# Optimization experiments

Measured on AMD Instinct MI355X. Metric: run time of the kernel, lower is better.

The kernel has to match this reference:

```python
import jax, jax.numpy as jnp
import numpy as np

B, T, D = 16, 4096, 768
S_MAX = 128  # max sentence (segment) count per sample


def setup_inputs() -> dict:
    key = jax.random.key(0)
    ks = jax.random.split(key, 8)
    hidden = jax.random.normal(ks[0], (B, T, D), dtype=jnp.float32)
    # sorted per-token segment ids == cumulative torch.split span structure
    seg_ids = jnp.sort(jax.random.randint(ks[1], (B, T), 0, S_MAX, dtype=jnp.int32), axis=-1)
    s1, s2, s3 = 1.0 / np.sqrt(D), 1.0 / np.sqrt(384), 1.0 / np.sqrt(128)
    W1 = jax.random.normal(ks[2], (D, 384), dtype=jnp.float32) * s1
    b1 = jnp.zeros((384,), dtype=jnp.float32)
    W2 = jax.random.normal(ks[3], (384, 128), dtype=jnp.float32) * s2
    b2 = jnp.zeros((128,), dtype=jnp.float32)
    W3 = jax.random.normal(ks[4], (128, 2), dtype=jnp.float32) * s3
    b3 = jnp.zeros((2,), dtype=jnp.float32)
    return {"hidden": hidden, "seg_ids": seg_ids, "W1": W1, "b1": b1,
            "W2": W2, "b2": b2, "W3": W3, "b3": b3}


def reference(hidden, seg_ids, W1, b1, W2, b2, W3, b3):
    # split_tensor: per-sample segment-sum over token spans, padded to S_MAX.
    # Segments with no tokens come out zero, matching F.pad of the torch code.
    sent_em = jax.vmap(
        lambda h, s: jax.ops.segment_sum(h, s, num_segments=S_MAX)
    )(hidden, seg_ids)  # [B, S_MAX, D]
    # sent_pred MLP head
    x = jax.nn.relu(jnp.einsum('bsd,df->bsf', sent_em, W1) + b1)
    x = jax.nn.relu(jnp.einsum('bsf,fg->bsg', x, W2) + b2)
    pred = jnp.einsum('bsg,gc->bsc', x, W3) + b3  # [B, S_MAX, 2]
    return pred.reshape(B * S_MAX, -1)
```

## Files before the change

### kernel.cpp

```cpp
#include <hip/hip_runtime.h>

#define BATCH 16
#define TOK   4096
#define DIM   768
#define SMAX  128
#define BM    8

typedef float f32x4 __attribute__((ext_vector_type(4)));
typedef short s16x8 __attribute__((ext_vector_type(8)));

__device__ __forceinline__ int lower_bound_i(const int* __restrict__ a, int n, int v) {
    int lo = 0, hi = n;
    while (lo < hi) {
        int m = (lo + hi) >> 1;
        if (a[m] < v) lo = m + 1; else hi = m;
    }
    return lo;
}

__device__ __forceinline__ float f4get(const float4& v, int k) {
    switch (k) {
        case 0: return v.x;
        case 1: return v.y;
        case 2: return v.z;
        default: return v.w;
    }
}

__device__ __forceinline__ void f4acc(float4& a, const float4& v) {
    a.x += v.x; a.y += v.y; a.z += v.z; a.w += v.w;
}

__device__ __forceinline__ unsigned short bf16_rne(float f) {
    unsigned int u = __float_as_uint(f);
    u += 0x7FFFu + ((u >> 16) & 1u);
    return (unsigned short)(u >> 16);
}

__device__ __forceinline__ unsigned int bf16_pack2(float f0, float f1) {
    unsigned int u0 = __float_as_uint(f0) + 0x8000u;
    unsigned int u1 = __float_as_uint(f1) + 0x8000u;
    return (u0 >> 16) | (u1 & 0xFFFF0000u);
}

__global__ __launch_bounds__(768)
void prep_w1t_kernel(const float* __restrict__ W1, unsigned short* __restrict__ W1T) {
    const int c = blockIdx.x;
    const int k = threadIdx.x;
    W1T[c * 768 + k] = bf16_rne(W1[(size_t)k * 384 + c]);
}

__global__ __launch_bounds__(192)
void bounds_kernel(const int* __restrict__ seg, int* __restrict__ bounds) {
    const int b = blockIdx.x;
    const int s = threadIdx.x;
    if (s <= SMAX)
        bounds[b * (SMAX + 1) + s] = lower_bound_i(seg + b * TOK, TOK, s);
}

__global__ __launch_bounds__(1024)
void fused_kernel(const float* __restrict__ hidden,
                  const int* __restrict__ bounds,
                  const unsigned short* __restrict__ W1T, const float* __restrict__ b1,
                  const float* __restrict__ W2, const float* __restrict__ b2,
                  const float* __restrict__ W3, const float* __restrict__ b3,
                  float* __restrict__ out) {
    __shared__ __align__(16) unsigned int A_bf32[16 * 388];
    __shared__ __align__(16) float X1[BM * 384];
    __shared__ __align__(16) float X2[BM * 128];
    __shared__ __align__(16) float P2[8 * BM * 128];

    const int tid  = threadIdx.x;
    const int row0 = blockIdx.x * BM;
    const int b    = row0 / SMAX;
    const int s0   = row0 % SMAX;
    const int grp  = tid >> 7;
    const int lane = tid & 127;
    const int h    = lane >> 6;
    const int l6   = lane & 63;

    for (int i = tid; i < 8 * 388; i += 1024)
        A_bf32[8 * 388 + i] = 0u;

    {
        const int lo = bounds[b * (SMAX + 1) + s0 + grp];
        const int hi = bounds[b * (SMAX + 1) + s0 + grp + 1];

        const float4* __restrict__ hp =
            reinterpret_cast<const float4*>(hidden + (size_t)b * TOK * DIM) + l6 * 3;

        float4 a0 = make_float4(0.f, 0.f, 0.f, 0.f);
        float4 a1 = make_float4(0.f, 0.f, 0.f, 0.f);
        float4 a2 = make_float4(0.f, 0.f, 0.f, 0.f);

        int t = lo + h;
        for (; t + 8 <= hi; t += 8) {
            float4 v0[4], v1[4], v2[4];
            #pragma unroll
            for (int u = 0; u < 4; ++u) {
                const float4* p = hp + (size_t)(t + 2 * u) * 192;
                v0[u] = p[0]; v1[u] = p[1]; v2[u] = p[2];
            }
            #pragma unroll
            for (int u = 0; u < 4; ++u) {
                f4acc(a0, v0[u]); f4acc(a1, v1[u]); f4acc(a2, v2[u]);
            }
        }
        for (; t < hi; t += 2) {
            const float4* p = hp + (size_t)t * 192;
            f4acc(a0, p[0]); f4acc(a1, p[1]); f4acc(a2, p[2]);
        }

        float4* scr = reinterpret_cast<float4*>(P2) + (grp * 64 + l6) * 3;
        if (h == 1) {
            scr[0] = a0; scr[1] = a1; scr[2] = a2;
        }
        __syncthreads();
        if (h == 0) {
            f4acc(a0, scr[0]); f4acc(a1, scr[1]); f4acc(a2, scr[2]);
            const int base = grp * 388 + l6 * 6;
            A_bf32[base + 0] = bf16_pack2(a0.x, a0.y);
            A_bf32[base + 1] = bf16_pack2(a0.z, a0.w);
            A_bf32[base + 2] = bf16_pack2(a1.x, a1.y);
            A_bf32[base + 3] = bf16_pack2(a1.z, a1.w);
            A_bf32[base + 4] = bf16_pack2(a2.x, a2.y);
            A_bf32[base + 5] = bf16_pack2(a2.z, a2.w);
        }
    }
    __syncthreads();

    {
        const int wid  = tid >> 6;
        const int l    = tid & 63;
        const int lrow = l & 15;
        const int lg   = l >> 4;

        if (wid < 12) {
            const int n0 = wid * 32;
            const int n1 = n0 + 16;
            f32x4 acc0 = {0.f, 0.f, 0.f, 0.f};
            f32x4 acc1 = {0.f, 0.f, 0.f, 0.f};

            const unsigned int* abase = &A_bf32[lrow * 388 + lg * 4];
            const unsigned short* w0p = W1T + (size_t)(n0 + lrow) * 768 + lg * 8;
            const unsigned short* w1p = W1T + (size_t)(n1 + lrow) * 768 + lg * 8;

            for (int ks = 0; ks < 24; ++ks) {
                s16x8 af  = *reinterpret_cast<const s16x8*>(abase + ks * 16);
                s16x8 bf0 = *reinterpret_cast<const s16x8*>(w0p + ks * 32);
                s16x8 bf1 = *reinterpret_cast<const s16x8*>(w1p + ks * 32);
                acc0 = __builtin_amdgcn_mfma_f32_16x16x32_bf16(af, bf0, acc0, 0, 0, 0);
                acc1 = __builtin_amdgcn_mfma_f32_16x16x32_bf16(af, bf1, acc1, 0, 0, 0);
            }

            if (lg < 2) {
                const int c0  = n0 + lrow;
                const int c1c = n1 + lrow;
                const float bb0 = b1[c0];
                const float bb1 = b1[c1c];
                #pragma unroll
                for (int r4 = 0; r4 < 4; ++r4) {
                    const int row = lg * 4 + r4;
                    const float v0 = acc0[r4] + bb0;
                    const float v1 = acc1[r4] + bb1;
                    X1[row * 384 + c0]  = v0 > 0.f ? v0 : 0.f;
                    X1[row * 384 + c1c] = v1 > 0.f ? v1 : 0.f;
                }
            }
        }
    }
    __syncthreads();

    const int c1 = lane;
    const int kg = grp;
    {
        float acc2[BM];
        #pragma unroll
        for (int r = 0; r < BM; ++r) acc2[r] = 0.f;

        const int k0 = kg * 48;
        for (int k = k0; k < k0 + 48; k += 4) {
            float4 x[BM];
            #pragma unroll
            for (int r = 0; r < BM; ++r)
                x[r] = *reinterpret_cast<const float4*>(&X1[r * 384 + k]);
            #pragma unroll
            for (int kk = 0; kk < 4; ++kk) {
                const float w = W2[(size_t)(k + kk) * 128 + c1];
                #pragma unroll
                for (int r = 0; r < BM; ++r)
                    acc2[r] = fmaf(f4get(x[r], kk), w, acc2[r]);
            }
        }
        #pragma unroll
        for (int r = 0; r < BM; ++r)
            P2[(kg * BM + r) * 128 + c1] = acc2[r];
    }
    __syncthreads();

    {
        const int row = grp;
        const int col = c1;
        float s = b2[col];
        #pragma unroll
        for (int g = 0; g < 8; ++g)
            s += P2[(g * BM + row) * 128 + col];
        X2[row * 128 + col] = s > 0.f ? s : 0.f;
    }
    __syncthreads();

    if (tid < BM * 2) {
        const int r = tid >> 1;
        const int c = tid & 1;
        float sacc = 0.f;
        #pragma unroll 8
        for (int k = 0; k < 128; ++k)
            sacc = fmaf(X2[r * 128 + k], W3[k * 2 + c], sacc);
        out[(row0 + r) * 2 + c] = sacc + b3[c];
    }
}

extern "C" void kernel_launch(void* const* d_in, const int* in_sizes, int n_in,
                              void* d_out, int out_size, void* d_ws, size_t ws_size,
                              hipStream_t stream) {
    const float* hidden = (const float*)d_in[0];
    const int*   seg    = (const int*)d_in[1];
    const float* W1     = (const float*)d_in[2];
    const float* b1     = (const float*)d_in[3];
    const float* W2     = (const float*)d_in[4];
    const float* b2     = (const float*)d_in[5];
    const float* W3     = (const float*)d_in[6];
    const float* b3     = (const float*)d_in[7];
    float* out = (float*)d_out;

    int* bounds = (int*)d_ws;
    unsigned short* W1T = (unsigned short*)((char*)d_ws + 16384);

    prep_w1t_kernel<<<384, 768, 0, stream>>>(W1, W1T);
    bounds_kernel<<<BATCH, 192, 0, stream>>>(seg, bounds);
    fused_kernel<<<(BATCH * SMAX) / BM, 1024, 0, stream>>>(
        hidden, bounds, W1T, b1, W2, b2, W3, b3, out);
}
```

Baseline: 65.82 us.

## Halve rows per block to 4 with 512 threads, doubling grid size

Each fused block now handles 4 segments with 512 threads instead of 8 with 1024, which doubles the grid to 512 blocks. The MFMA stage is reworked so each of the 8 waves computes 48 output columns using three 16x16 MFMAs, with only 4 of 16 A rows live (the rest are zero padding). The layer-2 split-K partition is reduced from 8 to 4 groups, and the reduction scratch gets its own shared buffer. The goal is better spread across CUs and more overlap of the memory-bound segment sum, at the cost of reading the W1T and W2 weights twice as often overall and wasting more MFMA work on padding rows.

```diff
diff --git a/kernel.cpp b/kernel.cpp
--- a/kernel.cpp
+++ b/kernel.cpp
@@ -4,7 +4,7 @@
 #define TOK   4096
 #define DIM   768
 #define SMAX  128
-#define BM    8
+#define BM    4
 
 typedef float f32x4 __attribute__((ext_vector_type(4)));
 typedef short s16x8 __attribute__((ext_vector_type(8)));
@@ -58,7 +58,7 @@
         bounds[b * (SMAX + 1) + s] = lower_bound_i(seg + b * TOK, TOK, s);
 }
 
-__global__ __launch_bounds__(1024)
+__global__ __launch_bounds__(512)
 void fused_kernel(const float* __restrict__ hidden,
                   const int* __restrict__ bounds,
                   const unsigned short* __restrict__ W1T, const float* __restrict__ b1,
@@ -68,7 +68,8 @@
     __shared__ __align__(16) unsigned int A_bf32[16 * 388];
     __shared__ __align__(16) float X1[BM * 384];
     __shared__ __align__(16) float X2[BM * 128];
-    __shared__ __align__(16) float P2[8 * BM * 128];
+    __shared__ __align__(16) float P2[4 * BM * 128];
+    __shared__ __align__(16) float4 SCR[4 * 64 * 3];
 
     const int tid  = threadIdx.x;
     const int row0 = blockIdx.x * BM;
@@ -79,8 +80,8 @@
     const int h    = lane >> 6;
     const int l6   = lane & 63;
 
-    for (int i = tid; i < 8 * 388; i += 1024)
-        A_bf32[8 * 388 + i] = 0u;
+    for (int i = tid; i < 12 * 388; i += 512)
+        A_bf32[4 * 388 + i] = 0u;
 
     {
         const int lo = bounds[b * (SMAX + 1) + s0 + grp];
@@ -111,7 +112,7 @@
             f4acc(a0, p[0]); f4acc(a1, p[1]); f4acc(a2, p[2]);
         }
 
-        float4* scr = reinterpret_cast<float4*>(P2) + (grp * 64 + l6) * 3;
+        float4* scr = &SCR[(grp * 64 + l6) * 3];
         if (h == 1) {
             scr[0] = a0; scr[1] = a1; scr[2] = a2;
         }
@@ -135,36 +136,33 @@
         const int lrow = l & 15;
         const int lg   = l >> 4;
 
-        if (wid < 12) {
-            const int n0 = wid * 32;
-            const int n1 = n0 + 16;
-            f32x4 acc0 = {0.f, 0.f, 0.f, 0.f};
-            f32x4 acc1 = {0.f, 0.f, 0.f, 0.f};
-
-            const unsigned int* abase = &A_bf32[lrow * 388 + lg * 4];
-            const unsigned short* w0p = W1T + (size_t)(n0 + lrow) * 768 + lg * 8;
-            const unsigned short* w1p = W1T + (size_t)(n1 + lrow) * 768 + lg * 8;
-
-            for (int ks = 0; ks < 24; ++ks) {
-                s16x8 af  = *reinterpret_cast<const s16x8*>(abase + ks * 16);
-                s16x8 bf0 = *reinterpret_cast<const s16x8*>(w0p + ks * 32);
-                s16x8 bf1 = *reinterpret_cast<const s16x8*>(w1p + ks * 32);
-                acc0 = __builtin_amdgcn_mfma_f32_16x16x32_bf16(af, bf0, acc0, 0, 0, 0);
-                acc1 = __builtin_amdgcn_mfma_f32_16x16x32_bf16(af, bf1, acc1, 0, 0, 0);
-            }
-
-            if (lg < 2) {
-                const int c0  = n0 + lrow;
-                const int c1c = n1 + lrow;
-                const float bb0 = b1[c0];
-                const float bb1 = b1[c1c];
+        const int nb = wid * 48;
+        f32x4 acc[3] = {{0.f,0.f,0.f,0.f},{0.f,0.f,0.f,0.f},{0.f,0.f,0.f,0.f}};
+
+        const unsigned int* abase = &A_bf32[lrow * 388 + lg * 4];
+        const unsigned short* wp[3];
+        #pragma unroll
+        for (int j = 0; j < 3; ++j)
+            wp[j] = W1T + (size_t)(nb + j * 16 + lrow) * 768 + lg * 8;
+
+        for (int ks = 0; ks < 24; ++ks) {
+            s16x8 af = *reinterpret_cast<const s16x8*>(abase + ks * 16);
+            #pragma unroll
+            for (int j = 0; j < 3; ++j) {
+                s16x8 bf = *reinterpret_cast<const s16x8*>(wp[j] + ks * 32);
+                acc[j] = __builtin_amdgcn_mfma_f32_16x16x32_bf16(af, bf, acc[j], 0, 0, 0);
+            }
+        }
+
+        if (lg == 0) {
+            #pragma unroll
+            for (int j = 0; j < 3; ++j) {
+                const int c = nb + j * 16 + lrow;
+                const float bb = b1[c];
                 #pragma unroll
                 for (int r4 = 0; r4 < 4; ++r4) {
-                    const int row = lg * 4 + r4;
-                    const float v0 = acc0[r4] + bb0;
-                    const float v1 = acc1[r4] + bb1;
-                    X1[row * 384 + c0]  = v0 > 0.f ? v0 : 0.f;
-                    X1[row * 384 + c1c] = v1 > 0.f ? v1 : 0.f;
+                    const float v = acc[j][r4] + bb;
+                    X1[r4 * 384 + c] = v > 0.f ? v : 0.f;
                 }
             }
         }
@@ -178,8 +176,8 @@
         #pragma unroll
         for (int r = 0; r < BM; ++r) acc2[r] = 0.f;
 
-        const int k0 = kg * 48;
-        for (int k = k0; k < k0 + 48; k += 4) {
+        const int k0 = kg * 96;
+        for (int k = k0; k < k0 + 96; k += 4) {
             float4 x[BM];
             #pragma unroll
             for (int r = 0; r < BM; ++r)
@@ -203,7 +201,7 @@
         const int col = c1;
         float s = b2[col];
         #pragma unroll
-        for (int g = 0; g < 8; ++g)
+        for (int g = 0; g < 4; ++g)
             s += P2[(g * BM + row) * 128 + col];
         X2[row * 128 + col] = s > 0.f ? s : 0.f;
     }
@@ -238,6 +236,6 @@
 
     prep_w1t_kernel<<<384, 768, 0, stream>>>(W1, W1T);
     bounds_kernel<<<BATCH, 192, 0, stream>>>(seg, bounds);
-    fused_kernel<<<(BATCH * SMAX) / BM, 1024, 0, stream>>>(
+    fused_kernel<<<(BATCH * SMAX) / BM, 512, 0, stream>>>(
         hidden, bounds, W1T, b1, W2, b2, W3, b3, out);
 }
```

New measurement: 78.33 us. 19.0% more time.

## Split segment-sum into separate per-segment kernel feeding bf16 MLP kernel

Applied to the files above, without the earlier changes.

Moves the segment-sum out of the fused kernel into its own kernel with one 192-thread block per (segment, batch). Each block streams hidden rows with deep unrolled float4 loads and writes the bf16-packed sentence embedding to workspace. The MLP kernel then just loads these packed rows into LDS. The aim is more blocks and more loads in flight for the memory-bound reduction (2048 small blocks instead of 256 large ones). The cost is an extra launch and a round trip of the intermediate through global memory.

```diff
diff --git a/kernel.cpp b/kernel.cpp
--- a/kernel.cpp
+++ b/kernel.cpp
@@ -58,13 +58,56 @@
         bounds[b * (SMAX + 1) + s] = lower_bound_i(seg + b * TOK, TOK, s);
 }
 
+__global__ __launch_bounds__(192)
+void segsum_bf16_kernel(const float* __restrict__ hidden,
+                        const int* __restrict__ bounds,
+                        unsigned int* __restrict__ sentb) {
+    const int s = blockIdx.x;
+    const int b = blockIdx.y;
+    const int tid = threadIdx.x;
+
+    const int lo = bounds[b * (SMAX + 1) + s];
+    const int hi = bounds[b * (SMAX + 1) + s + 1];
+
+    const float4* __restrict__ hp =
+        reinterpret_cast<const float4*>(hidden + (size_t)b * TOK * DIM) + tid;
+
+    float4 acc = make_float4(0.f, 0.f, 0.f, 0.f);
+    int t = lo;
+
+    for (; t + 16 <= hi; t += 16) {
+        float4 v[16];
+        #pragma unroll
+        for (int u = 0; u < 16; ++u)
+            v[u] = hp[(size_t)(t + u) * (DIM / 4)];
+        #pragma unroll
+        for (int u = 0; u < 16; ++u)
+            f4acc(acc, v[u]);
+    }
+    for (; t + 4 <= hi; t += 4) {
+        float4 v[4];
+        #pragma unroll
+        for (int u = 0; u < 4; ++u)
+            v[u] = hp[(size_t)(t + u) * (DIM / 4)];
+        #pragma unroll
+        for (int u = 0; u < 4; ++u)
+            f4acc(acc, v[u]);
+    }
+    for (; t < hi; ++t)
+        f4acc(acc, hp[(size_t)t * (DIM / 4)]);
+
+    uint2 pk;
+    pk.x = bf16_pack2(acc.x, acc.y);
+    pk.y = bf16_pack2(acc.z, acc.w);
+    reinterpret_cast<uint2*>(sentb + (size_t)(b * SMAX + s) * 384)[tid] = pk;
+}
+
 __global__ __launch_bounds__(1024)
-void fused_kernel(const float* __restrict__ hidden,
-                  const int* __restrict__ bounds,
-                  const unsigned short* __restrict__ W1T, const float* __restrict__ b1,
-                  const float* __restrict__ W2, const float* __restrict__ b2,
-                  const float* __restrict__ W3, const float* __restrict__ b3,
-                  float* __restrict__ out) {
+void mlp_kernel(const unsigned int* __restrict__ sentb,
+                const unsigned short* __restrict__ W1T, const float* __restrict__ b1,
+                const float* __restrict__ W2, const float* __restrict__ b2,
+                const float* __restrict__ W3, const float* __restrict__ b3,
+                float* __restrict__ out) {
     __shared__ __align__(16) unsigned int A_bf32[16 * 388];
     __shared__ __align__(16) float X1[BM * 384];
     __shared__ __align__(16) float X2[BM * 128];
@@ -72,60 +115,20 @@
 
     const int tid  = threadIdx.x;
     const int row0 = blockIdx.x * BM;
-    const int b    = row0 / SMAX;
-    const int s0   = row0 % SMAX;
     const int grp  = tid >> 7;
     const int lane = tid & 127;
-    const int h    = lane >> 6;
-    const int l6   = lane & 63;
-
-    for (int i = tid; i < 8 * 388; i += 1024)
-        A_bf32[8 * 388 + i] = 0u;
-
-    {
-        const int lo = bounds[b * (SMAX + 1) + s0 + grp];
-        const int hi = bounds[b * (SMAX + 1) + s0 + grp + 1];
-
-        const float4* __restrict__ hp =
-            reinterpret_cast<const float4*>(hidden + (size_t)b * TOK * DIM) + l6 * 3;
-
-        float4 a0 = make_float4(0.f, 0.f, 0.f, 0.f);
-        float4 a1 = make_float4(0.f, 0.f, 0.f, 0.f);
-        float4 a2 = make_float4(0.f, 0.f, 0.f, 0.f);
-
-        int t = lo + h;
-        for (; t + 8 <= hi; t += 8) {
-            float4 v0[4], v1[4], v2[4];
-            #pragma unroll
-            for (int u = 0; u < 4; ++u) {
-                const float4* p = hp + (size_t)(t + 2 * u) * 192;
-                v0[u] = p[0]; v1[u] = p[1]; v2[u] = p[2];
-            }
-            #pragma unroll
-            for (int u = 0; u < 4; ++u) {
-                f4acc(a0, v0[u]); f4acc(a1, v1[u]); f4acc(a2, v2[u]);
-            }
+
+    {
+        const unsigned int* src = sentb + (size_t)row0 * 384;
+        #pragma unroll
+        for (int i = 0; i < 3; ++i) {
+            const int idx = tid + i * 1024;
+            const int row = idx / 384;
+            const int col = idx - row * 384;
+            A_bf32[row * 388 + col] = src[idx];
         }
-        for (; t < hi; t += 2) {
-            const float4* p = hp + (size_t)t * 192;
-            f4acc(a0, p[0]); f4acc(a1, p[1]); f4acc(a2, p[2]);
-        }
-
-        float4* scr = reinterpret_cast<float4*>(P2) + (grp * 64 + l6) * 3;
-        if (h == 1) {
-            scr[0] = a0; scr[1] = a1; scr[2] = a2;
-        }
-        __syncthreads();
-        if (h == 0) {
-            f4acc(a0, scr[0]); f4acc(a1, scr[1]); f4acc(a2, scr[2]);
-            const int base = grp * 388 + l6 * 6;
-            A_bf32[base + 0] = bf16_pack2(a0.x, a0.y);
-            A_bf32[base + 1] = bf16_pack2(a0.z, a0.w);
-            A_bf32[base + 2] = bf16_pack2(a1.x, a1.y);
-            A_bf32[base + 3] = bf16_pack2(a1.z, a1.w);
-            A_bf32[base + 4] = bf16_pack2(a2.x, a2.y);
-            A_bf32[base + 5] = bf16_pack2(a2.z, a2.w);
-        }
+        for (int i = tid; i < 8 * 388; i += 1024)
+            A_bf32[8 * 388 + i] = 0u;
     }
     __syncthreads();
 
@@ -235,9 +238,11 @@
 
     int* bounds = (int*)d_ws;
     unsigned short* W1T = (unsigned short*)((char*)d_ws + 16384);
+    unsigned int* sentb = (unsigned int*)((char*)d_ws + 16384 + 589824 + 1024);
 
     prep_w1t_kernel<<<384, 768, 0, stream>>>(W1, W1T);
     bounds_kernel<<<BATCH, 192, 0, stream>>>(seg, bounds);
-    fused_kernel<<<(BATCH * SMAX) / BM, 1024, 0, stream>>>(
-        hidden, bounds, W1T, b1, W2, b2, W3, b3, out);
-}
+    segsum_bf16_kernel<<<dim3(SMAX, BATCH), 192, 0, stream>>>(hidden, bounds, sentb);
+    mlp_kernel<<<(BATCH * SMAX) / BM, 1024, 0, stream>>>(
+        sentb, W1T, b1, W2, b2, W3, b3, out);
+}
```

Result: slower. 70.17 us (+6.6%).
